# Kernel tuning notes

Hardware: AMD Instinct MI355X
Metric: run time of the kernel (lower is better)

Reference implementation:

```python
import jax, jax.numpy as jnp
import numpy as np

EPS = 1e-6
LAM = 0.005


def setup_inputs() -> dict:
    key = jax.random.key(0)
    k1, k2, k3 = jax.random.split(key, 3)
    B, D, H, W, M = 16, 256, 128, 128, 4096
    z = jax.random.normal(k1, (B, D, H, W), dtype=jnp.float32)
    z_prime = jax.random.normal(k2, (B, D, H, W), dtype=jnp.float32)
    # Precomputed sampled pixel indices (flat over H*W). With randn inputs every
    # pixel passes the validity mask, so uniform sampling matches the original.
    flat_idx = jax.random.randint(k3, (B, M), 0, H * W, dtype=jnp.int32)
    return {"z": z, "z_prime": z_prime, "flat_idx": flat_idx}


def _gather_pixels(z, flat_idx):
    # z: (B, D, H, W), flat_idx: (B, M) -> (B*M, D)
    B, D, H, W = z.shape
    M = flat_idx.shape[1]
    z_flat = z.reshape(B, D, H * W)
    g = jnp.take_along_axis(z_flat, flat_idx[:, None, :], axis=2)  # (B, D, M)
    return g.transpose(0, 2, 1).reshape(B * M, D)


def _normalise(x):
    mean = jnp.mean(x, axis=0, keepdims=True)
    std = jnp.std(x, axis=0, keepdims=True, ddof=1)  # torch .std() is unbiased
    return (x - mean) / jnp.clip(std, EPS, None)


def reference(z, z_prime, flat_idx):
    D = z.shape[1]
    zm = _normalise(_gather_pixels(z, flat_idx))        # (N, D)
    zpm = _normalise(_gather_pixels(z_prime, flat_idx))  # (N, D)
    N = zm.shape[0]
    C = (zm.T @ zpm) / N                                 # (D, D)
    on_diag = jnp.diagonal(C)
    off_diag = C.reshape(-1)[1:].reshape(D - 1, D + 1)[:, :-1]
    loss = jnp.sum((1.0 - on_diag) ** 2) + LAM * jnp.sum(off_diag ** 2)
    return loss
```

## Files before the change

kernel.cpp:

```cpp
#include <hip/hip_runtime.h>
#include <hip/hip_bf16.h>

typedef short s16x8 __attribute__((ext_vector_type(8)));
typedef float f32x16 __attribute__((ext_vector_type(16)));

namespace {
constexpr int kB = 16;
constexpr int kD = 256;
constexpr int kHW = 16384;
constexpr int kM = 4096;
constexpr int kN = kB * kM;
constexpr int kKChunk = 1024;
constexpr int kNChunks = kN / kKChunk;
constexpr float kLam = 0.005f;
}

__global__ __launch_bounds__(256) void gather_stats_kernel(
    const float* __restrict__ z, const float* __restrict__ zp,
    const int* __restrict__ flat_idx,
    __hip_bfloat16* __restrict__ Ag, __hip_bfloat16* __restrict__ Bg,
    float* __restrict__ Sp, float* __restrict__ SSp)
{
    __shared__ float plane[kHW];
    const int bx = blockIdx.x;
    const int sel = bx >> 12;
    const int b = (bx >> 8) & (kB - 1);
    const int d = bx & (kD - 1);
    const int t = threadIdx.x;

    const float* src = (sel ? zp : z) + ((size_t)(b * kD + d)) * kHW;
    const float4* s4 = (const float4*)src;
    float4* p4 = (float4*)plane;
#pragma unroll
    for (int i = 0; i < 16; ++i) p4[t + i * 256] = s4[t + i * 256];
    __syncthreads();

    const int* bi = flat_idx + b * kM;
    __hip_bfloat16* dst = (sel ? Bg : Ag) + (size_t)d * kN + b * kM;
    float s = 0.f, ss = 0.f;
#pragma unroll
    for (int i = 0; i < 16; ++i) {
        const int m = t + i * 256;
        const float v = plane[bi[m]];
        s += v;
        ss += v * v;
        dst[m] = __float2bfloat16(v);
    }
#pragma unroll
    for (int o = 32; o; o >>= 1) {
        s += __shfl_down(s, o);
        ss += __shfl_down(ss, o);
    }
    __syncthreads();
    if ((t & 63) == 0) {
        plane[t >> 6] = s;
        plane[4 + (t >> 6)] = ss;
    }
    __syncthreads();
    if (t == 0) {
        const int slot = (sel * kB + b) * kD + d;
        Sp[slot]  = plane[0] + plane[1] + plane[2] + plane[3];
        SSp[slot] = plane[4] + plane[5] + plane[6] + plane[7];
    }
}

__global__ __launch_bounds__(256) void gemm_part_kernel(
    const __hip_bfloat16* __restrict__ Ag, const __hip_bfloat16* __restrict__ Bg,
    float* __restrict__ partial)
{
    const int bx = blockIdx.x;
    const int tile = bx & 15;
    const int chunk = bx >> 4;
    const int tr = (tile >> 2) * 64;
    const int tc = (tile & 3) * 64;
    const int tid = threadIdx.x;
    const int wid = tid >> 6;
    const int lane = tid & 63;
    const int l31 = lane & 31;
    const int half = lane >> 5;
    const int d0 = tr + (wid >> 1) * 32;
    const int e0 = tc + (wid & 1) * 32;

    const __hip_bfloat16* arow = Ag + (size_t)(d0 + l31) * kN;
    const __hip_bfloat16* brow = Bg + (size_t)(e0 + l31) * kN;
    int kb = chunk * kKChunk + half * 8;

    f32x16 acc;
#pragma unroll
    for (int i = 0; i < 16; ++i) acc[i] = 0.f;

#pragma unroll 4
    for (int it = 0; it < kKChunk / 16; ++it) {
        s16x8 a = *(const s16x8*)(arow + kb);
        s16x8 bf = *(const s16x8*)(brow + kb);
        acc = __builtin_amdgcn_mfma_f32_32x32x16_bf16(a, bf, acc, 0, 0, 0);
        kb += 16;
    }

    float* out = partial + (size_t)chunk * (kD * kD);
#pragma unroll
    for (int r = 0; r < 16; ++r) {
        const int row = (r & 3) + 8 * (r >> 2) + 4 * half;
        out[(d0 + row) * kD + (e0 + l31)] = acc[r];
    }
}

__global__ __launch_bounds__(256) void reduce_gram_kernel(
    const float* __restrict__ partial, float* __restrict__ G)
{
    const int d = blockIdx.x;
    const int e = threadIdx.x;
    float s = 0.f;
#pragma unroll 8
    for (int c = 0; c < kNChunks; ++c)
        s += partial[(size_t)c * (kD * kD) + d * kD + e];
    G[d * kD + e] = s;
}

__global__ __launch_bounds__(256) void loss_kernel(
    const float* __restrict__ G, const float* __restrict__ Sp,
    const float* __restrict__ SSp, float* __restrict__ out)
{
    __shared__ float muA[kD], isA[kD], muB[kD], isB[kD];
    const int t = threadIdx.x;
    float sA = 0.f, ssA = 0.f, sB = 0.f, ssB = 0.f;
#pragma unroll
    for (int b = 0; b < kB; ++b) {
        sA  += Sp [(0 * kB + b) * kD + t];
        ssA += SSp[(0 * kB + b) * kD + t];
        sB  += Sp [(1 * kB + b) * kD + t];
        ssB += SSp[(1 * kB + b) * kD + t];
    }
    const float n = (float)kN;
    const float mA = sA / n, mB = sB / n;
    float vA = (ssA - n * mA * mA) / (n - 1.f);
    float vB = (ssB - n * mB * mB) / (n - 1.f);
    float sdA = fmaxf(sqrtf(fmaxf(vA, 0.f)), 1e-6f);
    float sdB = fmaxf(sqrtf(fmaxf(vB, 0.f)), 1e-6f);
    muA[t] = mA; isA[t] = 1.f / sdA;
    muB[t] = mB; isB[t] = 1.f / sdB;
    __syncthreads();

    float acc = 0.f;
    for (int d = 0; d < kD; ++d) {
        const int e = t;
        const float c = (G[d * kD + e] / n - muA[d] * muB[e]) * isA[d] * isB[e];
        if (d == e) { const float u = 1.f - c; acc += u * u; }
        else        { acc += kLam * c * c; }
    }
#pragma unroll
    for (int o = 32; o; o >>= 1) acc += __shfl_down(acc, o);
    __shared__ float r[4];
    if ((t & 63) == 0) r[t >> 6] = acc;
    __syncthreads();
    if (t == 0) out[0] = r[0] + r[1] + r[2] + r[3];
}

extern "C" void kernel_launch(void* const* d_in, const int* in_sizes, int n_in,
                              void* d_out, int out_size, void* d_ws, size_t ws_size,
                              hipStream_t stream) {
    const float* z  = (const float*)d_in[0];
    const float* zp = (const float*)d_in[1];
    const int* flat_idx = (const int*)d_in[2];
    float* out = (float*)d_out;

    char* ws = (char*)d_ws;
    __hip_bfloat16* Ag = (__hip_bfloat16*)ws;
    __hip_bfloat16* Bg = (__hip_bfloat16*)(ws + (size_t)32 * 1024 * 1024);
    float* partial = (float*)(ws + (size_t)64 * 1024 * 1024);
    float* Sp  = (float*)(ws + (size_t)80 * 1024 * 1024);
    float* SSp = Sp + 2 * kB * kD;
    float* G   = (float*)(ws + (size_t)80 * 1024 * 1024 + 64 * 1024);

    gather_stats_kernel<<<2 * kB * kD, 256, 0, stream>>>(z, zp, flat_idx, Ag, Bg, Sp, SSp);
    gemm_part_kernel<<<16 * kNChunks, 256, 0, stream>>>(Ag, Bg, partial);
    reduce_gram_kernel<<<kD, 256, 0, stream>>>(partial, G);
    loss_kernel<<<1, 256, 0, stream>>>(G, Sp, SSp, out);
}
```

Before: 216.4 us.

## Replace gather with per-pixel count histogram and fuse weighted Gram with stats

Instead of gathering sampled pixels into bf16 matrices, a new count kernel builds a per-batch histogram of how often each pixel was sampled. A fused kernel then streams every pixel of z and z' once and computes the Gram matrix as a count-weighted sum, along with weighted sums and sums of squares for the statistics. This removes the scattered gather and the intermediate bf16 writes and re-reads. In exchange it reads all 16384 pixels instead of 4096 samples, does four times the MFMA work, and writes 256 partial Gram matrices that a separate reduction kernel must sum.

```diff
diff --git a/kernel.cpp b/kernel.cpp
--- a/kernel.cpp
+++ b/kernel.cpp
@@ -10,98 +10,160 @@
 constexpr int kHW = 16384;
 constexpr int kM = 4096;
 constexpr int kN = kB * kM;
-constexpr int kKChunk = 1024;
-constexpr int kNChunks = kN / kKChunk;
+constexpr int kWin = 1024;
+constexpr int kNBlk = kB * (kHW / kWin);
 constexpr float kLam = 0.005f;
-}
-
-__global__ __launch_bounds__(256) void gather_stats_kernel(
+
+__device__ __forceinline__ unsigned short f2bf(float f) {
+    union { float f; unsigned u; } x{f};
+    const unsigned r = x.u + 0x7FFFu + ((x.u >> 16) & 1u);
+    return (unsigned short)(r >> 16);
+}
+}
+
+__global__ __launch_bounds__(256) void count_kernel(
+    const int* __restrict__ flat_idx, int* __restrict__ cnt)
+{
+    __shared__ int h[kHW];
+    const int t = threadIdx.x;
+    const int b = blockIdx.x;
+    for (int i = t; i < kHW; i += 256) h[i] = 0;
+    __syncthreads();
+    const int* bi = flat_idx + b * kM;
+    for (int i = t; i < kM; i += 256) atomicAdd(&h[bi[i]], 1);
+    __syncthreads();
+    int* dst = cnt + b * kHW;
+    for (int i = t; i < kHW; i += 256) dst[i] = h[i];
+}
+
+__global__ __launch_bounds__(512, 2) void fused_gram_kernel(
     const float* __restrict__ z, const float* __restrict__ zp,
-    const int* __restrict__ flat_idx,
-    __hip_bfloat16* __restrict__ Ag, __hip_bfloat16* __restrict__ Bg,
-    float* __restrict__ Sp, float* __restrict__ SSp)
-{
-    __shared__ float plane[kHW];
+    const int* __restrict__ cnt,
+    float* __restrict__ partial, float* __restrict__ statsPart)
+{
+    __shared__ char smem[65536];
+    __hip_bfloat16* As = (__hip_bfloat16*)smem;
+    __hip_bfloat16* Bs = (__hip_bfloat16*)(smem + 32768);
+
     const int bx = blockIdx.x;
-    const int sel = bx >> 12;
-    const int b = (bx >> 8) & (kB - 1);
-    const int d = bx & (kD - 1);
+    const int b = bx & (kB - 1);
+    const int win0 = (bx >> 4) * kWin;
     const int t = threadIdx.x;
-
-    const float* src = (sel ? zp : z) + ((size_t)(b * kD + d)) * kHW;
-    const float4* s4 = (const float4*)src;
-    float4* p4 = (float4*)plane;
-#pragma unroll
-    for (int i = 0; i < 16; ++i) p4[t + i * 256] = s4[t + i * 256];
-    __syncthreads();
-
-    const int* bi = flat_idx + b * kM;
-    __hip_bfloat16* dst = (sel ? Bg : Ag) + (size_t)d * kN + b * kM;
-    float s = 0.f, ss = 0.f;
-#pragma unroll
-    for (int i = 0; i < 16; ++i) {
-        const int m = t + i * 256;
-        const float v = plane[bi[m]];
-        s += v;
-        ss += v * v;
-        dst[m] = __float2bfloat16(v);
-    }
-#pragma unroll
-    for (int o = 32; o; o >>= 1) {
-        s += __shfl_down(s, o);
-        ss += __shfl_down(ss, o);
-    }
-    __syncthreads();
-    if ((t & 63) == 0) {
-        plane[t >> 6] = s;
-        plane[4 + (t >> 6)] = ss;
-    }
-    __syncthreads();
-    if (t == 0) {
-        const int slot = (sel * kB + b) * kD + d;
-        Sp[slot]  = plane[0] + plane[1] + plane[2] + plane[3];
-        SSp[slot] = plane[4] + plane[5] + plane[6] + plane[7];
-    }
-}
-
-__global__ __launch_bounds__(256) void gemm_part_kernel(
-    const __hip_bfloat16* __restrict__ Ag, const __hip_bfloat16* __restrict__ Bg,
-    float* __restrict__ partial)
-{
-    const int bx = blockIdx.x;
-    const int tile = bx & 15;
-    const int chunk = bx >> 4;
-    const int tr = (tile >> 2) * 64;
-    const int tc = (tile & 3) * 64;
-    const int tid = threadIdx.x;
-    const int wid = tid >> 6;
-    const int lane = tid & 63;
+    const int w = t >> 6;
+    const int lane = t & 63;
     const int l31 = lane & 31;
     const int half = lane >> 5;
-    const int d0 = tr + (wid >> 1) * 32;
-    const int e0 = tc + (wid & 1) * 32;
-
-    const __hip_bfloat16* arow = Ag + (size_t)(d0 + l31) * kN;
-    const __hip_bfloat16* brow = Bg + (size_t)(e0 + l31) * kN;
-    int kb = chunk * kKChunk + half * 8;
-
-    f32x16 acc;
-#pragma unroll
-    for (int i = 0; i < 16; ++i) acc[i] = 0.f;
-
-#pragma unroll 4
-    for (int it = 0; it < kKChunk / 16; ++it) {
-        s16x8 a = *(const s16x8*)(arow + kb);
-        s16x8 bf = *(const s16x8*)(brow + kb);
-        acc = __builtin_amdgcn_mfma_f32_32x32x16_bf16(a, bf, acc, 0, 0, 0);
-        kb += 16;
-    }
-
-    float* out = partial + (size_t)chunk * (kD * kD);
-#pragma unroll
-    for (int r = 0; r < 16; ++r) {
-        const int row = (r & 3) + 8 * (r >> 2) + 4 * half;
-        out[(d0 + row) * kD + (e0 + l31)] = acc[r];
+    const int wr = w >> 2;
+    const int wc = w & 3;
+
+    const int rbase = t >> 4;
+    const int cg = t & 15;
+
+    const float* zb  = z  + (size_t)b * kD * kHW;
+    const float* zpb = zp + (size_t)b * kD * kHW;
+    const int* cb = cnt + b * kHW;
+
+    f32x16 acc[4][2];
+#pragma unroll
+    for (int i = 0; i < 4; ++i)
+#pragma unroll
+        for (int j = 0; j < 2; ++j)
+#pragma unroll
+            for (int r = 0; r < 16; ++r) acc[i][j][r] = 0.f;
+
+    float sA[8], ssA[8], sB[8], ssB[8];
+#pragma unroll
+    for (int q = 0; q < 8; ++q) { sA[q] = ssA[q] = sB[q] = ssB[q] = 0.f; }
+
+    for (int kt = 0; kt < kWin / 64; ++kt) {
+        const int p0 = win0 + kt * 64;
+        const int4 ci = *(const int4*)(cb + p0 + cg * 4);
+        const float cf[4] = {(float)ci.x, (float)ci.y, (float)ci.z, (float)ci.w};
+
+#pragma unroll
+        for (int q = 0; q < 8; ++q) {
+            const int r = 32 * q + rbase;
+            const size_t goff = (size_t)r * kHW + p0 + cg * 4;
+            const float4 vA = *(const float4*)(zb + goff);
+            const float4 vB = *(const float4*)(zpb + goff);
+            const float a[4] = {vA.x, vA.y, vA.z, vA.w};
+            const float bb[4] = {vB.x, vB.y, vB.z, vB.w};
+            ushort4 pa, pb;
+            unsigned short* pav = (unsigned short*)&pa;
+            unsigned short* pbv = (unsigned short*)&pb;
+#pragma unroll
+            for (int j = 0; j < 4; ++j) {
+                const float wa = cf[j] * a[j];
+                const float wb = cf[j] * bb[j];
+                sA[q] += wa; ssA[q] += wa * a[j];
+                sB[q] += wb; ssB[q] += wb * bb[j];
+                pav[j] = f2bf(a[j]);
+                pbv[j] = f2bf(wb);
+            }
+            const int off = r * 128 + (((cg >> 1) ^ (r & 7)) << 4) + ((cg & 1) << 3);
+            *(ushort4*)(smem + off) = pa;
+            *(ushort4*)(smem + 32768 + off) = pb;
+        }
+        __syncthreads();
+
+#pragma unroll
+        for (int ks = 0; ks < 4; ++ks) {
+            s16x8 af[4], bf[2];
+#pragma unroll
+            for (int rt = 0; rt < 4; ++rt) {
+                const int row = 128 * wr + 32 * rt + l31;
+                const int slot = (2 * ks + half) ^ (row & 7);
+                af[rt] = *(const s16x8*)(smem + row * 128 + slot * 16);
+            }
+#pragma unroll
+            for (int ct = 0; ct < 2; ++ct) {
+                const int row = 64 * wc + 32 * ct + l31;
+                const int slot = (2 * ks + half) ^ (row & 7);
+                bf[ct] = *(const s16x8*)(smem + 32768 + row * 128 + slot * 16);
+            }
+#pragma unroll
+            for (int rt = 0; rt < 4; ++rt)
+#pragma unroll
+                for (int ct = 0; ct < 2; ++ct)
+                    acc[rt][ct] = __builtin_amdgcn_mfma_f32_32x32x16_bf16(
+                        af[rt], bf[ct], acc[rt][ct], 0, 0, 0);
+        }
+        __syncthreads();
+    }
+
+    float* out = partial + (size_t)bx * (kD * kD);
+#pragma unroll
+    for (int rt = 0; rt < 4; ++rt)
+#pragma unroll
+        for (int ct = 0; ct < 2; ++ct)
+#pragma unroll
+            for (int r = 0; r < 16; ++r) {
+                const int row = 128 * wr + 32 * rt + (r & 3) + 8 * (r >> 2) + 4 * half;
+                const int col = 64 * wc + 32 * ct + l31;
+                out[row * kD + col] = acc[rt][ct][r];
+            }
+
+    float* sd = (float*)smem;
+    __syncthreads();
+#pragma unroll
+    for (int q = 0; q < 8; ++q) {
+        const int row = 32 * q + rbase;
+        float* p = sd + (row * 16 + cg) * 4;
+        p[0] = sA[q]; p[1] = ssA[q]; p[2] = sB[q]; p[3] = ssB[q];
+    }
+    __syncthreads();
+    {
+        const int row = t >> 1;
+        const int pair = t & 1;
+        float a0 = 0.f, a1 = 0.f;
+#pragma unroll
+        for (int g = 0; g < 16; ++g) {
+            a0 += sd[(row * 16 + g) * 4 + 2 * pair];
+            a1 += sd[(row * 16 + g) * 4 + 2 * pair + 1];
+        }
+        float* p = statsPart + ((size_t)bx * kD + row) * 4;
+        p[2 * pair] = a0;
+        p[2 * pair + 1] = a1;
     }
 }
 
@@ -112,31 +174,28 @@
     const int e = threadIdx.x;
     float s = 0.f;
 #pragma unroll 8
-    for (int c = 0; c < kNChunks; ++c)
+    for (int c = 0; c < kNBlk; ++c)
         s += partial[(size_t)c * (kD * kD) + d * kD + e];
     G[d * kD + e] = s;
 }
 
 __global__ __launch_bounds__(256) void loss_kernel(
-    const float* __restrict__ G, const float* __restrict__ Sp,
-    const float* __restrict__ SSp, float* __restrict__ out)
+    const float* __restrict__ G, const float* __restrict__ statsPart,
+    float* __restrict__ out)
 {
     __shared__ float muA[kD], isA[kD], muB[kD], isB[kD];
     const int t = threadIdx.x;
     float sA = 0.f, ssA = 0.f, sB = 0.f, ssB = 0.f;
-#pragma unroll
-    for (int b = 0; b < kB; ++b) {
-        sA  += Sp [(0 * kB + b) * kD + t];
-        ssA += SSp[(0 * kB + b) * kD + t];
-        sB  += Sp [(1 * kB + b) * kD + t];
-        ssB += SSp[(1 * kB + b) * kD + t];
+    for (int blk = 0; blk < kNBlk; ++blk) {
+        const float4 v = *(const float4*)(statsPart + ((size_t)blk * kD + t) * 4);
+        sA += v.x; ssA += v.y; sB += v.z; ssB += v.w;
     }
     const float n = (float)kN;
     const float mA = sA / n, mB = sB / n;
-    float vA = (ssA - n * mA * mA) / (n - 1.f);
-    float vB = (ssB - n * mB * mB) / (n - 1.f);
-    float sdA = fmaxf(sqrtf(fmaxf(vA, 0.f)), 1e-6f);
-    float sdB = fmaxf(sqrtf(fmaxf(vB, 0.f)), 1e-6f);
+    const float vA = (ssA - n * mA * mA) / (n - 1.f);
+    const float vB = (ssB - n * mB * mB) / (n - 1.f);
+    const float sdA = fmaxf(sqrtf(fmaxf(vA, 0.f)), 1e-6f);
+    const float sdB = fmaxf(sqrtf(fmaxf(vB, 0.f)), 1e-6f);
     muA[t] = mA; isA[t] = 1.f / sdA;
     muB[t] = mB; isB[t] = 1.f / sdB;
     __syncthreads();
@@ -165,15 +224,13 @@
     float* out = (float*)d_out;
 
     char* ws = (char*)d_ws;
-    __hip_bfloat16* Ag = (__hip_bfloat16*)ws;
-    __hip_bfloat16* Bg = (__hip_bfloat16*)(ws + (size_t)32 * 1024 * 1024);
-    float* partial = (float*)(ws + (size_t)64 * 1024 * 1024);
-    float* Sp  = (float*)(ws + (size_t)80 * 1024 * 1024);
-    float* SSp = Sp + 2 * kB * kD;
-    float* G   = (float*)(ws + (size_t)80 * 1024 * 1024 + 64 * 1024);
-
-    gather_stats_kernel<<<2 * kB * kD, 256, 0, stream>>>(z, zp, flat_idx, Ag, Bg, Sp, SSp);
-    gemm_part_kernel<<<16 * kNChunks, 256, 0, stream>>>(Ag, Bg, partial);
+    int* cnt = (int*)ws;
+    float* statsPart = (float*)(ws + (size_t)1 * 1024 * 1024);
+    float* G = (float*)(ws + (size_t)2 * 1024 * 1024);
+    float* partial = (float*)(ws + (size_t)16 * 1024 * 1024);
+
+    count_kernel<<<kB, 256, 0, stream>>>(flat_idx, cnt);
+    fused_gram_kernel<<<kNBlk, 512, 0, stream>>>(z, zp, cnt, partial, statsPart);
     reduce_gram_kernel<<<kD, 256, 0, stream>>>(partial, G);
-    loss_kernel<<<1, 256, 0, stream>>>(G, Sp, SSp, out);
-}
+    loss_kernel<<<1, 256, 0, stream>>>(G, statsPart, out);
+}
```

New measurement: 252.8 us. 16.8% more time.
